# Optimization experiments

Measured on AMD Instinct MI355X. Metric: run time of the kernel, lower is better.

The kernel has to match this reference:

```python
import jax, jax.numpy as jnp
import numpy as np
from jax import lax

X_LB, X_UB = -1.0, 1.0
B, T, IN, H, OUT = 256, 16384, 1, 16, 1


def _rnn_layer(x, h0, Wih, Whh, bih, bhh):
    # x: [B, T, F], h0: [B, H] -> y: [B, T, H]  (tanh vanilla RNN)
    def step(h, xt):
        h = jnp.tanh(xt @ Wih.T + bih + h @ Whh.T + bhh)
        return h, h
    _, ys = lax.scan(step, h0, jnp.swapaxes(x, 0, 1))  # scan over time
    return jnp.swapaxes(ys, 0, 1)


def setup_inputs() -> dict:
    key = jax.random.key(0)
    ks = jax.random.split(key, 16)
    k = 1.0 / np.sqrt(H)  # torch nn.RNN init scale
    u = lambda kk, shape, s=k: jax.random.uniform(kk, shape, jnp.float32, -s, s)
    return {
        "x": jax.random.normal(ks[0], (B, T, IN), jnp.float32),
        "prev_h0": jax.random.normal(ks[1], (2, H), jnp.float32),
        "post_h0": jax.random.normal(ks[2], (1, OUT), jnp.float32),
        "W_ih0": u(ks[3], (H, IN)), "W_hh0": u(ks[4], (H, H)),
        "b_ih0": u(ks[5], (H,)), "b_hh0": u(ks[6], (H,)),
        "W_ih1": u(ks[7], (H, H)), "W_hh1": u(ks[8], (H, H)),
        "b_ih1": u(ks[9], (H,)), "b_hh1": u(ks[10], (H,)),
        "W_ihp": u(ks[11], (OUT, H), 1.0), "W_hhp": u(ks[12], (OUT, OUT), 1.0),
        "b_ihp": u(ks[13], (OUT,), 1.0), "b_hhp": u(ks[14], (OUT,), 1.0),
    }


def reference(x, prev_h0, post_h0, W_ih0, W_hh0, b_ih0, b_hh0,
              W_ih1, W_hh1, b_ih1, b_hh1, W_ihp, W_hhp, b_ihp, b_hhp):
    b = x.shape[0]
    xn = (x - X_LB) / (X_UB - X_LB)  # min-max normalization
    h0_l0 = jnp.broadcast_to(prev_h0[0], (b, H))
    h0_l1 = jnp.broadcast_to(prev_h0[1], (b, H))
    h0_p = jnp.broadcast_to(post_h0[0], (b, OUT))
    y = _rnn_layer(xn, h0_l0, W_ih0, W_hh0, b_ih0, b_hh0)
    y = _rnn_layer(y, h0_l1, W_ih1, W_hh1, b_ih1, b_hh1)
    y = _rnn_layer(y, h0_p, W_ihp, W_hhp, b_ihp, b_hhp)
    return y
```

## Files before the change

### kernel.cpp

```cpp
#include <hip/hip_runtime.h>


#define T_LEN 16384
#define NBATCH 256
#define HDIM 16
#define SEG_LEN 128
#define WARMUP 64
#define NSEG (T_LEN / SEG_LEN)
#define KSC 2.88539008177793f

typedef __attribute__((ext_vector_type(8))) short short8;
typedef __attribute__((ext_vector_type(4))) float float4v;

#define MFMA(a, b, c) __builtin_amdgcn_mfma_f32_16x16x32_bf16(a, b, c, 0, 0, 0)

#define CSTR 48
#define P_H1HI 768
#define P_H0LO 1536
#define P_XT 3072
#define P_YT 4352
#define WS_STRIDE 5632

__device__ __forceinline__ float tanh_pre(float s) {
  float e = __builtin_amdgcn_exp2f(s);
  float r = __builtin_amdgcn_rcpf(e + 1.0f);
  return __builtin_fmaf(-2.0f, r, 1.0f);
}

__device__ __forceinline__ void write_hi(float4v d, char* hi) {
  uint2 hp;
  hp.x = __builtin_amdgcn_perm(__float_as_uint(d[1]), __float_as_uint(d[0]),
                               0x07060302u);
  hp.y = __builtin_amdgcn_perm(__float_as_uint(d[3]), __float_as_uint(d[2]),
                               0x07060302u);
  *(uint2*)hi = hp;
}

__device__ __forceinline__ void split_write(float4v d, char* hi, char* lo) {
  unsigned b0 = __float_as_uint(d[0]), b1 = __float_as_uint(d[1]);
  unsigned b2 = __float_as_uint(d[2]), b3 = __float_as_uint(d[3]);
  uint2 hp;
  hp.x = __builtin_amdgcn_perm(b1, b0, 0x07060302u);
  hp.y = __builtin_amdgcn_perm(b3, b2, 0x07060302u);
  float l0 = d[0] - __uint_as_float(b0 & 0xFFFF0000u);
  float l1 = d[1] - __uint_as_float(b1 & 0xFFFF0000u);
  float l2 = d[2] - __uint_as_float(b2 & 0xFFFF0000u);
  float l3 = d[3] - __uint_as_float(b3 & 0xFFFF0000u);
  uint2 lp;
  lp.x = __builtin_amdgcn_perm(__float_as_uint(l1), __float_as_uint(l0),
                               0x07060302u);
  lp.y = __builtin_amdgcn_perm(__float_as_uint(l3), __float_as_uint(l2),
                               0x07060302u);
  *(uint2*)hi = hp;
  *(uint2*)lo = lp;
}

__device__ __forceinline__ short bf16hi(float v) {
  return (short)(__float_as_uint(v) >> 16);
}

__global__ __launch_bounds__(256, 2) void rnn3_kernel(
    const float* __restrict__ x, const float* __restrict__ prev_h0,
    const float* __restrict__ post_h0, const float* __restrict__ Wih0,
    const float* __restrict__ Whh0, const float* __restrict__ bih0,
    const float* __restrict__ bhh0, const float* __restrict__ Wih1,
    const float* __restrict__ Whh1, const float* __restrict__ bih1,
    const float* __restrict__ bhh1, const float* __restrict__ Wihp,
    const float* __restrict__ Whhp, const float* __restrict__ bihp,
    const float* __restrict__ bhhp, float* __restrict__ out) {
  const int lane = threadIdx.x & 63;
  const int wave = threadIdx.x >> 6;
  const int b = lane & 15;
  const int q = lane >> 4;
  const int bg = blockIdx.x >> 5;
  const int seg = ((blockIdx.x & 31) << 2) | wave;
  const int batch = bg * 16 + b;

  const int t0 = (seg == 0) ? 0 : seg * SEG_LEN - WARMUP;
  const int trip = (seg == 0) ? SEG_LEN : SEG_LEN + WARMUP;
  const int wchunks = (seg == 0) ? 0 : WARMUP / 16;

  __shared__ char smem[4 * WS_STRIDE];
  char* ws = smem + wave * WS_STRIDE;
  char* wrH0 = ws + b * CSTR + q * 8;
  char* wrH1 = ws + P_H1HI + b * CSTR + q * 8;
  char* pB1 = ws + b * CSTR + (q & 1) * 16 + (q >> 1) * P_H1HI;
  char* pB4 = ws + b * CSTR + (q & 1) * 16 + (q >> 1) * P_H0LO;
  char* pXtW = ws + P_XT + b * 80 + q * 16;
  char* pXtR = ws + P_XT + b * 80;
  char* pYW = ws + P_YT + b * 80;
  char* pYR = ws + P_YT + b * 80 + q * 16;

  short8 A1h, A1l, A4h, A5l, Ap;
  {
    const float* s1 = (q < 2) ? Wih1 : Whh1;
    const int col0 = (q & 1) * 8;
#pragma unroll
    for (int i = 0; i < 8; ++i) {
      float w = KSC * s1[b * HDIM + col0 + i];
      unsigned hb = __float_as_uint(w) & 0xFFFF0000u;
      A1h[i] = (short)(hb >> 16);
      A1l[i] = bf16hi(w - __uint_as_float(hb));
      float w0 = KSC * Whh0[b * HDIM + col0 + i];
      unsigned hb0 = __float_as_uint(w0) & 0xFFFF0000u;
      A4h[i] = (short)(hb0 >> 16);
      A5l[i] = (q < 2) ? bf16hi(w0 - __uint_as_float(hb0)) : (short)0;
      float wpv = (b == 0 && q >= 2) ? KSC * Wihp[(q - 2) * 8 + i] : 0.0f;
      Ap[i] = bf16hi(wpv);
    }
  }

  float4v c1v, c0pv, a0pv;
#pragma unroll
  for (int r = 0; r < 4; ++r) {
    const int row = q * 4 + r;
    c1v[r] = KSC * (bih1[row] + bhh1[row]);
    float a0w = Wih0[row];
    a0pv[r] = KSC * 0.5f * a0w;
    c0pv[r] = KSC * __builtin_fmaf(0.5f, a0w, bih0[row] + bhh0[row]);
  }
  const float whp = KSC * Whhp[0];
  float4v cpv = {0.f, 0.f, 0.f, 0.f};
  cpv[0] = (q == 0) ? KSC * (bihp[0] + bhhp[0]) : 0.0f;

  float yv = post_h0[0];
  float yw[16];
#pragma unroll
  for (int s = 0; s < 16; ++s) yw[s] = 0.0f;

  const float* xb = x + (size_t)batch * T_LEN + t0;
  float* ob = out + (size_t)batch * T_LEN + t0;

  {
    float4v h0i, h1i;
#pragma unroll
    for (int r = 0; r < 4; ++r) {
      h0i[r] = prev_h0[q * 4 + r];
      h1i[r] = prev_h0[HDIM + q * 4 + r];
    }
    split_write(h0i, wrH0, wrH0 + P_H0LO);
    write_hi(h1i, wrH1);
  }
  __builtin_amdgcn_wave_barrier();
  short8 B1 = *(const short8*)pB1;
  short8 B4 = *(const short8*)pB4;

  const int NC = trip / 16;
  for (int c = 0; c < NC; ++c) {
    float4 xq = *(const float4*)(xb + c * 16 + q * 4);
    *(float4*)pXtW = xq;
    __builtin_amdgcn_wave_barrier();

#pragma unroll
    for (int i = 0; i < 16; ++i) {
      if (i == 2) {
        if (c > wchunks) {
          if (q == 0) {
#pragma unroll
            for (int r = 0; r < 4; ++r) {
              float4 v = {yw[r * 4], yw[r * 4 + 1], yw[r * 4 + 2],
                          yw[r * 4 + 3]};
              *(float4*)(pYW + r * 16) = v;
            }
          }
          __builtin_amdgcn_wave_barrier();
          float4 yo = *(const float4*)pYR;
          *(float4*)(ob + (c - 1) * 16 + q * 4) = yo;
        }
      }

      const bool first = (c == 0 && i == 0);
      float xcur = *(const float*)(pXtR + i * 4);
      float4v cx;
#pragma unroll
      for (int r = 0; r < 4; ++r)
        cx[r] = __builtin_fmaf(a0pv[r], xcur, c0pv[r]);

      float4v d1 = MFMA(A1h, B1, c1v);
      d1 = MFMA(A1l, B1, d1);
      float4v dp = MFMA(Ap, B1, cpv);
      float4v d0 = MFMA(A4h, B4, cx);
      d0 = MFMA(A5l, B4, d0);

      float4v hn1, hn0;
#pragma unroll
      for (int r = 0; r < 4; ++r) {
        hn1[r] = tanh_pre(d1[r]);
        hn0[r] = tanh_pre(d0[r]);
      }

      float yn = tanh_pre(__builtin_fmaf(whp, yv, dp[0]));
      if (i >= 2) {
        yv = yn;
      } else {
        if (c > 0) yv = yn;
      }
      yw[(i + 14) & 15] = yv;

      split_write(hn0, wrH0, wrH0 + P_H0LO);
      if (!first) write_hi(hn1, wrH1);
      __builtin_amdgcn_wave_barrier();
      B1 = *(const short8*)pB1;
      B4 = *(const short8*)pB4;
    }
  }

  {
    float4v d1 = MFMA(A1h, B1, c1v);
    d1 = MFMA(A1l, B1, d1);
    float4v dp = MFMA(Ap, B1, cpv);
    float4v hn1;
#pragma unroll
    for (int r = 0; r < 4; ++r) hn1[r] = tanh_pre(d1[r]);
    yv = tanh_pre(__builtin_fmaf(whp, yv, dp[0]));
    yw[14] = yv;
    write_hi(hn1, wrH1);
    __builtin_amdgcn_wave_barrier();
    B1 = *(const short8*)pB1;
    dp = MFMA(Ap, B1, cpv);
    yv = tanh_pre(__builtin_fmaf(whp, yv, dp[0]));
    yw[15] = yv;
    if (q == 0) {
#pragma unroll
      for (int r = 0; r < 4; ++r) {
        float4 v = {yw[r * 4], yw[r * 4 + 1], yw[r * 4 + 2], yw[r * 4 + 3]};
        *(float4*)(pYW + r * 16) = v;
      }
    }
    __builtin_amdgcn_wave_barrier();
    float4 yo = *(const float4*)pYR;
    *(float4*)(ob + (NC - 1) * 16 + q * 4) = yo;
  }
}

extern "C" void kernel_launch(void* const* d_in, const int* in_sizes, int n_in,
                              void* d_out, int out_size, void* d_ws,
                              size_t ws_size, hipStream_t stream) {
  const float* x = (const float*)d_in[0];
  const float* prev_h0 = (const float*)d_in[1];
  const float* post_h0 = (const float*)d_in[2];
  const float* Wih0 = (const float*)d_in[3];
  const float* Whh0 = (const float*)d_in[4];
  const float* bih0 = (const float*)d_in[5];
  const float* bhh0 = (const float*)d_in[6];
  const float* Wih1 = (const float*)d_in[7];
  const float* Whh1 = (const float*)d_in[8];
  const float* bih1 = (const float*)d_in[9];
  const float* bhh1 = (const float*)d_in[10];
  const float* Wihp = (const float*)d_in[11];
  const float* Whhp = (const float*)d_in[12];
  const float* bihp = (const float*)d_in[13];
  const float* bhhp = (const float*)d_in[14];
  float* out = (float*)d_out;

  rnn3_kernel<<<dim3(512), dim3(256), 0, stream>>>(
      x, prev_h0, post_h0, Wih0, Whh0, bih0, bhh0, Wih1, Whh1, bih1, bhh1,
      Wihp, Whhp, bihp, bhhp, out);
}
```

Baseline: 165.6 us.

## Keep RNN hidden state in registers by permuting MFMA K layout, drop LDS

Reorders the K dimension of the weight A-operands so that each lane's own MFMA output rows form its B-operand. The recurrent hidden state can then be packed straight from registers into the next MFMA input, with no LDS round trip and no wave barrier per timestep. The x input is also loaded per lane straight from global memory, with the next chunk prefetched, and outputs are stored directly by q==0 lanes instead of being transposed through LDS. The price is redundant x loads across lanes and narrower output stores done by only one quarter of the lanes.

```diff
diff --git a/kernel.cpp b/kernel.cpp
--- a/kernel.cpp
+++ b/kernel.cpp
@@ -11,15 +11,9 @@
 
 typedef __attribute__((ext_vector_type(8))) short short8;
 typedef __attribute__((ext_vector_type(4))) float float4v;
+typedef __attribute__((ext_vector_type(4))) unsigned int uint4v;
 
 #define MFMA(a, b, c) __builtin_amdgcn_mfma_f32_16x16x32_bf16(a, b, c, 0, 0, 0)
-
-#define CSTR 48
-#define P_H1HI 768
-#define P_H0LO 1536
-#define P_XT 3072
-#define P_YT 4352
-#define WS_STRIDE 5632
 
 __device__ __forceinline__ float tanh_pre(float s) {
   float e = __builtin_amdgcn_exp2f(s);
@@ -27,36 +21,48 @@
   return __builtin_fmaf(-2.0f, r, 1.0f);
 }
 
-__device__ __forceinline__ void write_hi(float4v d, char* hi) {
-  uint2 hp;
-  hp.x = __builtin_amdgcn_perm(__float_as_uint(d[1]), __float_as_uint(d[0]),
-                               0x07060302u);
-  hp.y = __builtin_amdgcn_perm(__float_as_uint(d[3]), __float_as_uint(d[2]),
-                               0x07060302u);
-  *(uint2*)hi = hp;
-}
-
-__device__ __forceinline__ void split_write(float4v d, char* hi, char* lo) {
-  unsigned b0 = __float_as_uint(d[0]), b1 = __float_as_uint(d[1]);
-  unsigned b2 = __float_as_uint(d[2]), b3 = __float_as_uint(d[3]);
-  uint2 hp;
-  hp.x = __builtin_amdgcn_perm(b1, b0, 0x07060302u);
-  hp.y = __builtin_amdgcn_perm(b3, b2, 0x07060302u);
-  float l0 = d[0] - __uint_as_float(b0 & 0xFFFF0000u);
-  float l1 = d[1] - __uint_as_float(b1 & 0xFFFF0000u);
-  float l2 = d[2] - __uint_as_float(b2 & 0xFFFF0000u);
-  float l3 = d[3] - __uint_as_float(b3 & 0xFFFF0000u);
-  uint2 lp;
-  lp.x = __builtin_amdgcn_perm(__float_as_uint(l1), __float_as_uint(l0),
-                               0x07060302u);
-  lp.y = __builtin_amdgcn_perm(__float_as_uint(l3), __float_as_uint(l2),
-                               0x07060302u);
-  *(uint2*)hi = hp;
-  *(uint2*)lo = lp;
-}
-
 __device__ __forceinline__ short bf16hi(float v) {
   return (short)(__float_as_uint(v) >> 16);
+}
+
+__device__ __forceinline__ uint2 pack_hi(float4v d) {
+  uint2 p;
+  p.x = __builtin_amdgcn_perm(__float_as_uint(d[1]), __float_as_uint(d[0]),
+                              0x07060302u);
+  p.y = __builtin_amdgcn_perm(__float_as_uint(d[3]), __float_as_uint(d[2]),
+                              0x07060302u);
+  return p;
+}
+
+__device__ __forceinline__ uint2 pack_lo(float4v d) {
+  float l0 = d[0] - __uint_as_float(__float_as_uint(d[0]) & 0xFFFF0000u);
+  float l1 = d[1] - __uint_as_float(__float_as_uint(d[1]) & 0xFFFF0000u);
+  float l2 = d[2] - __uint_as_float(__float_as_uint(d[2]) & 0xFFFF0000u);
+  float l3 = d[3] - __uint_as_float(__float_as_uint(d[3]) & 0xFFFF0000u);
+  uint2 p;
+  p.x = __builtin_amdgcn_perm(__float_as_uint(l1), __float_as_uint(l0),
+                              0x07060302u);
+  p.y = __builtin_amdgcn_perm(__float_as_uint(l3), __float_as_uint(l2),
+                              0x07060302u);
+  return p;
+}
+
+__device__ __forceinline__ uint4v mk4(uint2 a, uint2 b) {
+  uint4v t;
+  t[0] = a.x;
+  t[1] = a.y;
+  t[2] = b.x;
+  t[3] = b.y;
+  return t;
+}
+
+__device__ __forceinline__ short8 as_s8(uint4v u) {
+  union {
+    uint4v u;
+    short8 s;
+  } c;
+  c.u = u;
+  return c.s;
 }
 
 __global__ __launch_bounds__(256, 2) void rnn3_kernel(
@@ -80,34 +86,21 @@
   const int trip = (seg == 0) ? SEG_LEN : SEG_LEN + WARMUP;
   const int wchunks = (seg == 0) ? 0 : WARMUP / 16;
 
-  __shared__ char smem[4 * WS_STRIDE];
-  char* ws = smem + wave * WS_STRIDE;
-  char* wrH0 = ws + b * CSTR + q * 8;
-  char* wrH1 = ws + P_H1HI + b * CSTR + q * 8;
-  char* pB1 = ws + b * CSTR + (q & 1) * 16 + (q >> 1) * P_H1HI;
-  char* pB4 = ws + b * CSTR + (q & 1) * 16 + (q >> 1) * P_H0LO;
-  char* pXtW = ws + P_XT + b * 80 + q * 16;
-  char* pXtR = ws + P_XT + b * 80;
-  char* pYW = ws + P_YT + b * 80;
-  char* pYR = ws + P_YT + b * 80 + q * 16;
-
   short8 A1h, A1l, A4h, A5l, Ap;
-  {
-    const float* s1 = (q < 2) ? Wih1 : Whh1;
-    const int col0 = (q & 1) * 8;
-#pragma unroll
-    for (int i = 0; i < 8; ++i) {
-      float w = KSC * s1[b * HDIM + col0 + i];
-      unsigned hb = __float_as_uint(w) & 0xFFFF0000u;
-      A1h[i] = (short)(hb >> 16);
-      A1l[i] = bf16hi(w - __uint_as_float(hb));
-      float w0 = KSC * Whh0[b * HDIM + col0 + i];
-      unsigned hb0 = __float_as_uint(w0) & 0xFFFF0000u;
-      A4h[i] = (short)(hb0 >> 16);
-      A5l[i] = (q < 2) ? bf16hi(w0 - __uint_as_float(hb0)) : (short)0;
-      float wpv = (b == 0 && q >= 2) ? KSC * Wihp[(q - 2) * 8 + i] : 0.0f;
-      Ap[i] = bf16hi(wpv);
-    }
+#pragma unroll
+  for (int i = 0; i < 8; ++i) {
+    const int r = 4 * q + (i & 3);
+    const float* s1 = (i < 4) ? Wih1 : Whh1;
+    float w1 = KSC * s1[b * HDIM + r];
+    unsigned hb = __float_as_uint(w1) & 0xFFFF0000u;
+    A1h[i] = (short)(hb >> 16);
+    A1l[i] = bf16hi(w1 - __uint_as_float(hb));
+    float w0 = KSC * Whh0[b * HDIM + r];
+    unsigned hb0 = __float_as_uint(w0) & 0xFFFF0000u;
+    A4h[i] = (short)(hb0 >> 16);
+    A5l[i] = (i < 4) ? bf16hi(w0 - __uint_as_float(hb0)) : (short)0;
+    float wpv = (b == 0 && i >= 4) ? KSC * Wihp[r] : 0.0f;
+    Ap[i] = bf16hi(wpv);
   }
 
   float4v c1v, c0pv, a0pv;
@@ -128,9 +121,10 @@
 #pragma unroll
   for (int s = 0; s < 16; ++s) yw[s] = 0.0f;
 
-  const float* xb = x + (size_t)batch * T_LEN + t0;
+  const float* xp = x + (size_t)batch * T_LEN + t0;
   float* ob = out + (size_t)batch * T_LEN + t0;
 
+  uint4v B4, B1;
   {
     float4v h0i, h1i;
 #pragma unroll
@@ -138,49 +132,59 @@
       h0i[r] = prev_h0[q * 4 + r];
       h1i[r] = prev_h0[HDIM + q * 4 + r];
     }
-    split_write(h0i, wrH0, wrH0 + P_H0LO);
-    write_hi(h1i, wrH1);
-  }
-  __builtin_amdgcn_wave_barrier();
-  short8 B1 = *(const short8*)pB1;
-  short8 B4 = *(const short8*)pB4;
+    uint2 h0h = pack_hi(h0i);
+    uint2 h0l = pack_lo(h0i);
+    uint2 h1h = pack_hi(h1i);
+    B4 = mk4(h0h, h0l);
+    B1 = mk4(h0h, h1h);
+  }
 
   const int NC = trip / 16;
+  float4v xA = *(const float4v*)(xp);
+  float4v xB = *(const float4v*)(xp + 4);
+  float4v xC = *(const float4v*)(xp + 8);
+  float4v xD = *(const float4v*)(xp + 12);
+
   for (int c = 0; c < NC; ++c) {
-    float4 xq = *(const float4*)(xb + c * 16 + q * 4);
-    *(float4*)pXtW = xq;
-    __builtin_amdgcn_wave_barrier();
+    float4v x0_ = xA, x1_ = xB, x2_ = xC, x3_ = xD;
+    if (c + 1 < NC) {
+      const float* xn = xp + (c + 1) * 16;
+      xA = *(const float4v*)(xn);
+      xB = *(const float4v*)(xn + 4);
+      xC = *(const float4v*)(xn + 8);
+      xD = *(const float4v*)(xn + 12);
+    }
 
 #pragma unroll
     for (int i = 0; i < 16; ++i) {
       if (i == 2) {
-        if (c > wchunks) {
-          if (q == 0) {
-#pragma unroll
-            for (int r = 0; r < 4; ++r) {
-              float4 v = {yw[r * 4], yw[r * 4 + 1], yw[r * 4 + 2],
-                          yw[r * 4 + 3]};
-              *(float4*)(pYW + r * 16) = v;
-            }
+        if (c > wchunks && q == 0) {
+#pragma unroll
+          for (int r = 0; r < 4; ++r) {
+            float4v v = {yw[r * 4], yw[r * 4 + 1], yw[r * 4 + 2],
+                         yw[r * 4 + 3]};
+            *(float4v*)(ob + (c - 1) * 16 + r * 4) = v;
           }
-          __builtin_amdgcn_wave_barrier();
-          float4 yo = *(const float4*)pYR;
-          *(float4*)(ob + (c - 1) * 16 + q * 4) = yo;
         }
       }
 
       const bool first = (c == 0 && i == 0);
-      float xcur = *(const float*)(pXtR + i * 4);
+      float xcur = (i < 4)    ? x0_[i & 3]
+                   : (i < 8)  ? x1_[i & 3]
+                   : (i < 12) ? x2_[i & 3]
+                              : x3_[i & 3];
       float4v cx;
 #pragma unroll
       for (int r = 0; r < 4; ++r)
         cx[r] = __builtin_fmaf(a0pv[r], xcur, c0pv[r]);
 
-      float4v d1 = MFMA(A1h, B1, c1v);
-      d1 = MFMA(A1l, B1, d1);
-      float4v dp = MFMA(Ap, B1, cpv);
-      float4v d0 = MFMA(A4h, B4, cx);
-      d0 = MFMA(A5l, B4, d0);
+      short8 B1s = as_s8(B1);
+      short8 B4s = as_s8(B4);
+      float4v d1 = MFMA(A1h, B1s, c1v);
+      d1 = MFMA(A1l, B1s, d1);
+      float4v dp = MFMA(Ap, B1s, cpv);
+      float4v d0 = MFMA(A4h, B4s, cx);
+      d0 = MFMA(A5l, B4s, d0);
 
       float4v hn1, hn0;
 #pragma unroll
@@ -197,39 +201,43 @@
       }
       yw[(i + 14) & 15] = yv;
 
-      split_write(hn0, wrH0, wrH0 + P_H0LO);
-      if (!first) write_hi(hn1, wrH1);
-      __builtin_amdgcn_wave_barrier();
-      B1 = *(const short8*)pB1;
-      B4 = *(const short8*)pB4;
+      uint2 h0h = pack_hi(hn0);
+      uint2 h0l = pack_lo(hn0);
+      B4 = mk4(h0h, h0l);
+      if (!first) {
+        uint2 h1h = pack_hi(hn1);
+        B1 = mk4(h0h, h1h);
+      } else {
+        B1[0] = h0h.x;
+        B1[1] = h0h.y;
+      }
     }
   }
 
   {
-    float4v d1 = MFMA(A1h, B1, c1v);
-    d1 = MFMA(A1l, B1, d1);
-    float4v dp = MFMA(Ap, B1, cpv);
+    short8 B1s = as_s8(B1);
+    float4v d1 = MFMA(A1h, B1s, c1v);
+    d1 = MFMA(A1l, B1s, d1);
+    float4v dp = MFMA(Ap, B1s, cpv);
     float4v hn1;
 #pragma unroll
     for (int r = 0; r < 4; ++r) hn1[r] = tanh_pre(d1[r]);
     yv = tanh_pre(__builtin_fmaf(whp, yv, dp[0]));
     yw[14] = yv;
-    write_hi(hn1, wrH1);
-    __builtin_amdgcn_wave_barrier();
-    B1 = *(const short8*)pB1;
-    dp = MFMA(Ap, B1, cpv);
+    uint2 h1h = pack_hi(hn1);
+    B1[2] = h1h.x;
+    B1[3] = h1h.y;
+    B1s = as_s8(B1);
+    dp = MFMA(Ap, B1s, cpv);
     yv = tanh_pre(__builtin_fmaf(whp, yv, dp[0]));
     yw[15] = yv;
     if (q == 0) {
 #pragma unroll
       for (int r = 0; r < 4; ++r) {
-        float4 v = {yw[r * 4], yw[r * 4 + 1], yw[r * 4 + 2], yw[r * 4 + 3]};
-        *(float4*)(pYW + r * 16) = v;
-      }
-    }
-    __builtin_amdgcn_wave_barrier();
-    float4 yo = *(const float4*)pYR;
-    *(float4*)(ob + (NC - 1) * 16 + q * 4) = yo;
+        float4v v = {yw[r * 4], yw[r * 4 + 1], yw[r * 4 + 2], yw[r * 4 + 3]};
+        *(float4v*)(ob + (NC - 1) * 16 + r * 4) = v;
+      }
+    }
   }
 }
 
```

Result: faster. 154.6 us (-6.6%).
